# Kernel tuning notes

Measured on AMD Instinct MI355X. Metric: run time of the kernel, lower is better.

## Reference

```python
import jax, jax.numpy as jnp
import numpy as np

M, K, N, GS = 64, 4096, 14336, 128
# pack() interleaves every block of 8 k-columns with perm [0,2,4,6,1,3,5,7];
# nibble i of a packed int32 holds original column 8*c + PERM[i].
PERM = np.array([0, 2, 4, 6, 1, 3, 5, 7])
INV_PERM = np.argsort(PERM)  # [0,4,1,5,2,6,3,7]


def setup_inputs() -> dict:
    key = jax.random.key(0)
    k1, k2, k3 = jax.random.split(key, 3)
    x = jax.random.normal(k1, (M, K), dtype=jnp.float32)
    B_packed = jax.random.randint(k2, (N, K // 8), 0, 2147483647, dtype=jnp.int32)
    # positive per-group scales (typical magnitude for 4-bit symmetric quant)
    s = jax.random.uniform(k3, (K // GS, N), dtype=jnp.float32) * 0.02 + 1e-3
    return {"x": x, "B_packed": B_packed, "s": s}


def _dequantize(B_packed, s):
    # Unpack 8 nibbles per int32 -> (N, K//8, 8)
    u = B_packed.astype(jnp.uint32)
    nibs = jnp.stack([(u >> (4 * i)) & 0xF for i in range(8)], axis=-1)
    # Undo the pack-time column interleave within each block of 8
    nibs = nibs[..., jnp.asarray(INV_PERM)]
    q = nibs.reshape(N, K).astype(jnp.float32) - 8.0  # symmetric int4: values in [-8, 7]
    # Apply per-group, per-output-channel scales: s[k//GS, n]
    w = (q.reshape(N, K // GS, GS) * s.T[:, :, None]).reshape(N, K)  # (N, K)
    return w


def reference(x, B_packed, s):
    w = _dequantize(B_packed, s)        # (N, K) dequantized fp32 weight
    return jnp.einsum("mk,nk->mn", x, w)  # (M, N), no bias
```

## Files before the change

kernel.cpp:

```cpp
#include <hip/hip_runtime.h>
#include <stdint.h>

typedef _Float16 f16;
typedef f16   f16x2 __attribute__((ext_vector_type(2)));
typedef f16   f16x8 __attribute__((ext_vector_type(8)));
typedef float f32x4 __attribute__((ext_vector_type(4)));

static constexpr int M_ = 64;
static constexpr int K_ = 4096;
static constexpr int N_ = 14336;

__global__ void xconv_kernel(const float* __restrict__ x, uint4* __restrict__ xt) {
    int t = blockIdx.x * blockDim.x + threadIdx.x;
    int row = t >> 9, kb = t & 511;
    int kg = kb >> 2, h = kb & 3, mt = row >> 4, l16 = row & 15;
    int dst = (kg * 4 + mt) * 64 + h * 16 + l16;
    const float4* p = reinterpret_cast<const float4*>(x) + 2 * (size_t)t;
    float4 a = p[0], b = p[1];
    union { f16x8 h8; uint4 v; } z;
    z.h8[0] = (f16)a.x; z.h8[1] = (f16)a.y; z.h8[2] = (f16)a.z; z.h8[3] = (f16)a.w;
    z.h8[4] = (f16)b.x; z.h8[5] = (f16)b.y; z.h8[6] = (f16)b.z; z.h8[7] = (f16)b.w;
    xt[dst] = z.v;
}

__device__ __forceinline__ void gload_lds16(const void* g, void* l) {
    __builtin_amdgcn_global_load_lds(
        (const __attribute__((address_space(1))) void*)g,
        (__attribute__((address_space(3))) void*)l, 16, 0, 0);
}

__device__ __forceinline__ f16x8 dequant(uint u, f16x2 sc) {
    const f16 m = (f16)(-1032.0f);
    const f16x2 mc = {m, m};
    union { f16x2 h2; uint uu; } um;
    union { f16x2 h2[4]; f16x8 v; } ob;
    #pragma unroll
    for (int p = 0; p < 4; ++p) {
        um.uu = 0x64006400u | ((u >> (4 * p)) & 0x000F000Fu);
        ob.h2[p] = (um.h2 + mc) * sc;
    }
    return ob.v;
}

template<bool PRE>
__global__ __launch_bounds__(512, 4)
void gemm_kernel(const float* __restrict__ xf, const f16x8* __restrict__ xt,
                 const uint* __restrict__ bpk, const float* __restrict__ s,
                 float* __restrict__ out)
{
    __shared__ __align__(16) uint lbs[16384];
    const int lane = threadIdx.x & 63;
    const int w    = threadIdx.x >> 6;
    const int h    = lane >> 4;
    const int l16  = lane & 15;
    const int n0   = blockIdx.x * 32;

    f16x2 spk[4][2];
    #pragma unroll
    for (int g = 0; g < 4; ++g)
        #pragma unroll
        for (int nt = 0; nt < 2; ++nt) {
            float sv = s[(size_t)(w * 4 + g) * N_ + n0 + nt * 16 + l16];
            f16 sh = (f16)sv;
            spk[g][nt] = f16x2{sh, sh};
        }

    #pragma unroll
    for (int gl = 0; gl < 4; ++gl) {
        const int gdw = w * 64 + gl * 16 + h * 4;
        gload_lds16(bpk + (size_t)(n0 +      l16) * 512 + gdw, &lbs[w * 2048 + gl * 512]);
        gload_lds16(bpk + (size_t)(n0 + 16 + l16) * 512 + gdw, &lbs[w * 2048 + gl * 512 + 256]);
    }

    const f16x8* aw = xt + (size_t)w * 4096 + lane;
    auto loadA = [&](int g, int t, int mt) -> f16x8 {
        if constexpr (PRE) {
            return aw[((g * 4 + t) * 4 + mt) * 64];
        } else {
            const float* xp = xf + (size_t)(mt * 16 + l16) * K_ + (size_t)(w * 64 + g * 16 + t * 4 + h) * 8;
            float4 f0 = *reinterpret_cast<const float4*>(xp);
            float4 f1 = *reinterpret_cast<const float4*>(xp + 4);
            f16x8 av;
            av[0] = (f16)f0.x; av[1] = (f16)f0.y; av[2] = (f16)f0.z; av[3] = (f16)f0.w;
            av[4] = (f16)f1.x; av[5] = (f16)f1.y; av[6] = (f16)f1.z; av[7] = (f16)f1.w;
            return av;
        }
    };

    f16x8 a[2][4];
    #pragma unroll
    for (int mt = 0; mt < 4; ++mt) a[0][mt] = loadA(0, 0, mt);
    if constexpr (PRE) {
        asm volatile("s_waitcnt vmcnt(4)" ::: "memory");
    } else {
        asm volatile("s_waitcnt vmcnt(0)" ::: "memory");
    }
    __builtin_amdgcn_sched_barrier(0);

    f32x4 acc[2][4];
    #pragma unroll
    for (int nt = 0; nt < 2; ++nt)
        #pragma unroll
        for (int mt = 0; mt < 4; ++mt) acc[nt][mt] = f32x4{0.f, 0.f, 0.f, 0.f};

    #pragma unroll
    for (int g = 0; g < 4; ++g) {
        #pragma unroll
        for (int t = 0; t < 4; ++t) {
            const int st = g * 4 + t;
            if (st < 15) {
                const int gn = (st + 1) >> 2, tn = (st + 1) & 3;
                #pragma unroll
                for (int mt = 0; mt < 4; ++mt) a[(t + 1) & 1][mt] = loadA(gn, tn, mt);
            }
            const int bbase = w * 2048 + g * 512 + t * 64 + l16 * 4 + h;
            const uint u0 = lbs[bbase];
            const uint u1 = lbs[bbase + 256];
            const f16x8 b0 = dequant(u0, spk[g][0]);
            const f16x8 b1 = dequant(u1, spk[g][1]);
            #pragma unroll
            for (int mt = 0; mt < 4; ++mt)
                acc[0][mt] = __builtin_amdgcn_mfma_f32_16x16x32_f16(a[t & 1][mt], b0, acc[0][mt], 0, 0, 0);
            #pragma unroll
            for (int mt = 0; mt < 4; ++mt)
                acc[1][mt] = __builtin_amdgcn_mfma_f32_16x16x32_f16(a[t & 1][mt], b1, acc[1][mt], 0, 0, 0);
        }
    }

    f32x4* red = reinterpret_cast<f32x4*>(lbs);
    __syncthreads();
    if (w >= 4) {
        #pragma unroll
        for (int nt = 0; nt < 2; ++nt)
            #pragma unroll
            for (int mt = 0; mt < 4; ++mt)
                red[((w - 4) * 8 + nt * 4 + mt) * 64 + lane] = acc[nt][mt];
    }
    __syncthreads();
    if (w < 4) {
        #pragma unroll
        for (int nt = 0; nt < 2; ++nt)
            #pragma unroll
            for (int mt = 0; mt < 4; ++mt)
                acc[nt][mt] += red[(w * 8 + nt * 4 + mt) * 64 + lane];
    }
    __syncthreads();
    if (w == 2 || w == 3) {
        #pragma unroll
        for (int nt = 0; nt < 2; ++nt)
            #pragma unroll
            for (int mt = 0; mt < 4; ++mt)
                red[((w - 2) * 8 + nt * 4 + mt) * 64 + lane] = acc[nt][mt];
    }
    __syncthreads();
    if (w < 2) {
        #pragma unroll
        for (int nt = 0; nt < 2; ++nt)
            #pragma unroll
            for (int mt = 0; mt < 4; ++mt)
                acc[nt][mt] += red[(w * 8 + nt * 4 + mt) * 64 + lane];
    }
    __syncthreads();
    if (w < 2) {
        #pragma unroll
        for (int nt = 0; nt < 2; ++nt)
            #pragma unroll
            for (int mt = 0; mt < 4; ++mt)
                red[(w * 8 + nt * 4 + mt) * 64 + lane] = acc[nt][mt];
    }
    __syncthreads();
    {
        const int slot = w;
        f32x4 v = red[slot * 64 + lane];
        v += red[(8 + slot) * 64 + lane];
        const int nt = slot >> 2, mt = slot & 3;
        #pragma unroll
        for (int q = 0; q < 4; ++q)
            out[(size_t)(mt * 16 + h * 4 + q) * N_ + (n0 + nt * 16 + l16)] = v[q];
    }
}

extern "C" void kernel_launch(void* const* d_in, const int* in_sizes, int n_in,
                              void* d_out, int out_size, void* d_ws, size_t ws_size,
                              hipStream_t stream) {
    const float* x   = (const float*)d_in[0];
    const uint*  bpk = (const uint*)d_in[1];
    const float* s   = (const float*)d_in[2];
    float*       out = (float*)d_out;

    if (ws_size >= (size_t)(M_ * K_ * 2)) {
        xconv_kernel<<<128, 256, 0, stream>>>(x, (uint4*)d_ws);
        gemm_kernel<true><<<448, 512, 0, stream>>>(x, (const f16x8*)d_ws, bpk, s, out);
    } else {
        gemm_kernel<false><<<448, 512, 0, stream>>>(x, nullptr, bpk, s, out);
    }
}
```

Baseline: 27.47 us.

## Stage activations cooperatively through double-buffered LDS with register-prefetched weights

Replaces the per-wave private activation loads and the up-front weight copy into LDS with a 16-step K loop. In each step the whole block cooperatively loads an activation chunk into registers, writes it to a double-buffered LDS tile and shares it across waves. Weights and scales are prefetched directly into registers two steps ahead. This cuts redundant activation traffic per wave and spreads the weight load across the loop, at the cost of a block barrier and LDS round trip in every iteration.

```diff
diff --git a/kernel.cpp b/kernel.cpp
--- a/kernel.cpp
+++ b/kernel.cpp
@@ -23,12 +23,6 @@
     xt[dst] = z.v;
 }
 
-__device__ __forceinline__ void gload_lds16(const void* g, void* l) {
-    __builtin_amdgcn_global_load_lds(
-        (const __attribute__((address_space(1))) void*)g,
-        (__attribute__((address_space(3))) void*)l, 16, 0, 0);
-}
-
 __device__ __forceinline__ f16x8 dequant(uint u, f16x2 sc) {
     const f16 m = (f16)(-1032.0f);
     const f16x2 mc = {m, m};
@@ -44,57 +38,62 @@
 
 template<bool PRE>
 __global__ __launch_bounds__(512, 4)
-void gemm_kernel(const float* __restrict__ xf, const f16x8* __restrict__ xt,
+void gemm_kernel(const float* __restrict__ xf, const uint4* __restrict__ xt4,
                  const uint* __restrict__ bpk, const float* __restrict__ s,
                  float* __restrict__ out)
 {
     __shared__ __align__(16) uint lbs[16384];
-    const int lane = threadIdx.x & 63;
-    const int w    = threadIdx.x >> 6;
+    const int tid  = threadIdx.x;
+    const int lane = tid & 63;
+    const int w    = tid >> 6;
     const int h    = lane >> 4;
     const int l16  = lane & 15;
     const int n0   = blockIdx.x * 32;
 
-    f16x2 spk[4][2];
-    #pragma unroll
-    for (int g = 0; g < 4; ++g)
-        #pragma unroll
-        for (int nt = 0; nt < 2; ++nt) {
-            float sv = s[(size_t)(w * 4 + g) * N_ + n0 + nt * 16 + l16];
-            f16 sh = (f16)sv;
-            spk[g][nt] = f16x2{sh, sh};
+    auto loadA = [&](int c, uint4 r[4]) {
+        #pragma unroll
+        for (int q = 0; q < 4; ++q) {
+            if constexpr (PRE) {
+                r[q] = xt4[(size_t)c * 2048 + q * 512 + tid];
+            } else {
+                int slot = q * 512 + tid;
+                int kg = slot >> 8, rem = slot & 255;
+                int mt = rem >> 6, sub = rem & 63, hh = sub >> 4, ll = sub & 15;
+                const float* xp = xf + (size_t)(mt * 16 + ll) * K_ + (size_t)((c * 8 + kg) * 4 + hh) * 8;
+                float4 f0 = *reinterpret_cast<const float4*>(xp);
+                float4 f1 = *reinterpret_cast<const float4*>(xp + 4);
+                union { f16x8 h8; uint4 v; } ua;
+                ua.h8[0] = (f16)f0.x; ua.h8[1] = (f16)f0.y; ua.h8[2] = (f16)f0.z; ua.h8[3] = (f16)f0.w;
+                ua.h8[4] = (f16)f1.x; ua.h8[5] = (f16)f1.y; ua.h8[6] = (f16)f1.z; ua.h8[7] = (f16)f1.w;
+                r[q] = ua.v;
+            }
         }
-
-    #pragma unroll
-    for (int gl = 0; gl < 4; ++gl) {
-        const int gdw = w * 64 + gl * 16 + h * 4;
-        gload_lds16(bpk + (size_t)(n0 +      l16) * 512 + gdw, &lbs[w * 2048 + gl * 512]);
-        gload_lds16(bpk + (size_t)(n0 + 16 + l16) * 512 + gdw, &lbs[w * 2048 + gl * 512 + 256]);
-    }
-
-    const f16x8* aw = xt + (size_t)w * 4096 + lane;
-    auto loadA = [&](int g, int t, int mt) -> f16x8 {
-        if constexpr (PRE) {
-            return aw[((g * 4 + t) * 4 + mt) * 64];
-        } else {
-            const float* xp = xf + (size_t)(mt * 16 + l16) * K_ + (size_t)(w * 64 + g * 16 + t * 4 + h) * 8;
-            float4 f0 = *reinterpret_cast<const float4*>(xp);
-            float4 f1 = *reinterpret_cast<const float4*>(xp + 4);
-            f16x8 av;
-            av[0] = (f16)f0.x; av[1] = (f16)f0.y; av[2] = (f16)f0.z; av[3] = (f16)f0.w;
-            av[4] = (f16)f1.x; av[5] = (f16)f1.y; av[6] = (f16)f1.z; av[7] = (f16)f1.w;
-            return av;
-        }
-    };
-
-    f16x8 a[2][4];
-    #pragma unroll
-    for (int mt = 0; mt < 4; ++mt) a[0][mt] = loadA(0, 0, mt);
-    if constexpr (PRE) {
-        asm volatile("s_waitcnt vmcnt(4)" ::: "memory");
-    } else {
-        asm volatile("s_waitcnt vmcnt(0)" ::: "memory");
-    }
+    };
+    auto writeA = [&](int buf, const uint4 r[4]) {
+        uint4* dst = reinterpret_cast<uint4*>(lbs + buf * 8192);
+        #pragma unroll
+        for (int q = 0; q < 4; ++q) dst[q * 512 + tid] = r[q];
+    };
+    auto loadB = [&](int c, uint bo[2]) {
+        bo[0] = bpk[(size_t)(n0 +      l16) * 512 + c * 32 + w * 4 + h];
+        bo[1] = bpk[(size_t)(n0 + 16 + l16) * 512 + c * 32 + w * 4 + h];
+    };
+    auto loadS = [&](int c, float so[2]) {
+        const size_t g = (size_t)(2 * c + (w >> 2)) * N_;
+        so[0] = s[g + n0 + l16];
+        so[1] = s[g + n0 + 16 + l16];
+    };
+
+    uint4 ar[2][4];
+    uint  br[3][2];
+    float sf[3][2];
+    loadA(0, ar[0]); loadA(1, ar[1]);
+    loadB(0, br[0]); loadB(1, br[1]);
+    loadS(0, sf[0]); loadS(1, sf[1]);
+
+    writeA(0, ar[0]);
+    asm volatile("s_waitcnt lgkmcnt(0)" ::: "memory");
+    __builtin_amdgcn_s_barrier();
     __builtin_amdgcn_sched_barrier(0);
 
     f32x4 acc[2][4];
@@ -104,27 +103,33 @@
         for (int mt = 0; mt < 4; ++mt) acc[nt][mt] = f32x4{0.f, 0.f, 0.f, 0.f};
 
     #pragma unroll
-    for (int g = 0; g < 4; ++g) {
-        #pragma unroll
-        for (int t = 0; t < 4; ++t) {
-            const int st = g * 4 + t;
-            if (st < 15) {
-                const int gn = (st + 1) >> 2, tn = (st + 1) & 3;
-                #pragma unroll
-                for (int mt = 0; mt < 4; ++mt) a[(t + 1) & 1][mt] = loadA(gn, tn, mt);
-            }
-            const int bbase = w * 2048 + g * 512 + t * 64 + l16 * 4 + h;
-            const uint u0 = lbs[bbase];
-            const uint u1 = lbs[bbase + 256];
-            const f16x8 b0 = dequant(u0, spk[g][0]);
-            const f16x8 b1 = dequant(u1, spk[g][1]);
-            #pragma unroll
-            for (int mt = 0; mt < 4; ++mt)
-                acc[0][mt] = __builtin_amdgcn_mfma_f32_16x16x32_f16(a[t & 1][mt], b0, acc[0][mt], 0, 0, 0);
-            #pragma unroll
-            for (int mt = 0; mt < 4; ++mt)
-                acc[1][mt] = __builtin_amdgcn_mfma_f32_16x16x32_f16(a[t & 1][mt], b1, acc[1][mt], 0, 0, 0);
+    for (int c = 0; c < 16; ++c) {
+        if (c < 14) {
+            loadA(c + 2, ar[c & 1]);
+            loadB(c + 2, br[(c + 2) % 3]);
+            loadS(c + 2, sf[(c + 2) % 3]);
         }
+        if (c < 15) writeA((c + 1) & 1, ar[(c + 1) & 1]);
+
+        const f16x8* bufp = reinterpret_cast<const f16x8*>(lbs + (c & 1) * 8192);
+        f16x8 afr[4];
+        #pragma unroll
+        for (int mt = 0; mt < 4; ++mt)
+            afr[mt] = bufp[(w * 4 + mt) * 64 + h * 16 + l16];
+
+        const f16 s0 = (f16)sf[c % 3][0], s1 = (f16)sf[c % 3][1];
+        const f16x8 b0 = dequant(br[c % 3][0], f16x2{s0, s0});
+        const f16x8 b1 = dequant(br[c % 3][1], f16x2{s1, s1});
+        #pragma unroll
+        for (int mt = 0; mt < 4; ++mt)
+            acc[0][mt] = __builtin_amdgcn_mfma_f32_16x16x32_f16(afr[mt], b0, acc[0][mt], 0, 0, 0);
+        #pragma unroll
+        for (int mt = 0; mt < 4; ++mt)
+            acc[1][mt] = __builtin_amdgcn_mfma_f32_16x16x32_f16(afr[mt], b1, acc[1][mt], 0, 0, 0);
+
+        asm volatile("s_waitcnt lgkmcnt(0)" ::: "memory");
+        __builtin_amdgcn_s_barrier();
+        __builtin_amdgcn_sched_barrier(0);
     }
 
     f32x4* red = reinterpret_cast<f32x4*>(lbs);
@@ -190,7 +195,7 @@
 
     if (ws_size >= (size_t)(M_ * K_ * 2)) {
         xconv_kernel<<<128, 256, 0, stream>>>(x, (uint4*)d_ws);
-        gemm_kernel<true><<<448, 512, 0, stream>>>(x, (const f16x8*)d_ws, bpk, s, out);
+        gemm_kernel<true><<<448, 512, 0, stream>>>(x, (const uint4*)d_ws, bpk, s, out);
     } else {
         gemm_kernel<false><<<448, 512, 0, stream>>>(x, nullptr, bpk, s, out);
     }
```

Result: slower. 89.85 us (+227.1%).
